# Kernel optimization log

Measured on AMD Instinct MI355X. Metric: run time of the kernel, lower is better.

## Reference

```python
import jax, jax.numpy as jnp
import numpy as np

B, N, E, H = 2048, 256, 32, 64
DIN = N + 2 * E  # masked_x + self_emb + parent_emb


def _lin_init(k, fan_in, fan_out):
    return jax.random.normal(k, (fan_in, fan_out), jnp.float32) / np.sqrt(fan_in).astype(np.float32)


def setup_inputs() -> dict:
    key = jax.random.key(0)
    ks = jax.random.split(key, 8)
    return {
        "x": jax.random.normal(ks[0], (B, N), jnp.float32),
        "adjacency": jax.random.uniform(ks[1], (N, N), jnp.float32),
        "embeddings": 0.01 * jax.random.normal(ks[2], (N, E), jnp.float32),
        "W1": _lin_init(ks[3], DIN, H), "b1": jnp.zeros((H,), jnp.float32),
        "g1": jnp.ones((H,), jnp.float32), "bt1": jnp.zeros((H,), jnp.float32),
        "W2": _lin_init(ks[4], H, H), "b2": jnp.zeros((H,), jnp.float32),
        "g2": jnp.ones((H,), jnp.float32), "bt2": jnp.zeros((H,), jnp.float32),
        "W3": _lin_init(ks[5], H, 2), "b3": jnp.zeros((2,), jnp.float32),
    }


def _layernorm(h, g, b, eps=1e-5):
    m = h.mean(-1, keepdims=True)
    v = h.var(-1, keepdims=True)
    return (h - m) / jnp.sqrt(v + eps) * g + b


def _leaky_relu(h):
    return jnp.where(h >= 0, h, 0.2 * h)


def reference(x, adjacency, embeddings, W1, b1, g1, bt1, W2, b2, g2, bt2, W3, b3):
    b, n = x.shape
    e = embeddings.shape[1]
    # masked_x[b,i,j] = adjacency[j,i] * x[b,j]  (per-node parent masking, vectorized over i)
    masked = x[:, None, :] * adjacency.T[None, :, :]            # (B, N, N)
    self_emb = jnp.broadcast_to(embeddings[None], (b, n, e))    # (B, N, E)
    # parent_weights[:, i] = adjacency[:, i] / (sum + 1e-8); parent_emb_i = pw_i @ embeddings
    pw = adjacency / (adjacency.sum(axis=0, keepdims=True) + 1e-8)
    parent_emb = jnp.broadcast_to((pw.T @ embeddings)[None], (b, n, e))  # (B, N, E)
    inp = jnp.concatenate([masked, self_emb, parent_emb], axis=-1)       # (B, N, N+2E)
    h = _leaky_relu(_layernorm(inp @ W1 + b1, g1, bt1))
    h = _leaky_relu(_layernorm(h @ W2 + b2, g2, bt2))
    out = h @ W3 + b3                                            # (B, N, 2)
    return out[..., 0], out[..., 1]  # (means, log_stds), each (B, N)
```

## Files before the change

kernel.cpp:

```cpp
#include <hip/hip_runtime.h>
#include <hip/hip_bf16.h>

#define BB 2048
#define NN 256
#define EE 32
#define HH 64

typedef __attribute__((ext_vector_type(8))) short s16x8;
typedef __attribute__((ext_vector_type(4))) short s16x4;
typedef __attribute__((ext_vector_type(4))) float f32x4;

__device__ __forceinline__ unsigned short f32_to_bf16_rne(float f) {
    __hip_bfloat16 h = __float2bfloat16(f);
    return *reinterpret_cast<unsigned short*>(&h);
}
__device__ __forceinline__ float bf16_to_f32(unsigned short h) {
    return __uint_as_float(((unsigned int)h) << 16);
}

__global__ __launch_bounds__(256) void prep_all(
    const float* __restrict__ x, const float* __restrict__ A,
    const float* __restrict__ emb, const float* __restrict__ W1,
    const float* __restrict__ b1, const float* __restrict__ W2,
    unsigned short* __restrict__ xh, unsigned short* __restrict__ xl,
    unsigned short* __restrict__ w2h, unsigned short* __restrict__ w2l,
    float* __restrict__ c) {

    __shared__ float aS[NN];
    __shared__ float red[256];
    __shared__ float peS[EE];

    const int bid = blockIdx.x;
    const int t   = threadIdx.x;

    if (bid < 512) {
        const int i4 = (bid * 256 + t) * 4;
        const f32x4 v = *(const f32x4*)(x + i4);
        s16x4 hv, lv;
        #pragma unroll
        for (int q = 0; q < 4; ++q) {
            const unsigned short hb = f32_to_bf16_rne(v[q]);
            hv[q] = (short)hb;
            lv[q] = (short)f32_to_bf16_rne(v[q] - bf16_to_f32(hb));
        }
        *(s16x4*)(xh + i4) = hv;
        *(s16x4*)(xl + i4) = lv;
    } else if (bid < 528) {
        const int idx = (bid - 512) * 256 + t;
        const int n = idx >> 6, k = idx & 63;
        const float w = W2[k * HH + n];
        const unsigned short hb = f32_to_bf16_rne(w);
        w2h[n * HH + k] = hb;
        w2l[n * HH + k] = f32_to_bf16_rne(w - bf16_to_f32(hb));
    } else {
        const int i = bid - 528;
        const float a_t = A[t * NN + i];
        aS[t] = a_t;
        red[t] = a_t;
        __syncthreads();
        #pragma unroll
        for (int s = 128; s > 0; s >>= 1) {
            if (t < s) red[t] += red[t + s];
            __syncthreads();
        }
        const float inv = 1.f / (red[0] + 1e-8f);

        const int e = t & 31, jg = t >> 5;
        float part = 0.f;
        #pragma unroll 8
        for (int r = 0; r < 32; ++r) {
            const int j = jg * 32 + r;
            part = fmaf(aS[j], emb[j * EE + e], part);
        }
        __syncthreads();
        red[t] = part;
        __syncthreads();
        if (t < 32) {
            float pe = 0.f;
            #pragma unroll
            for (int g = 0; g < 8; ++g) pe += red[g * 32 + t];
            peS[t] = pe * inv;
        }
        __syncthreads();

        if (t < HH) {
            float ch = b1[t];
            const float* embi = emb + i * EE;
            #pragma unroll 8
            for (int e2 = 0; e2 < EE; ++e2) {
                ch = fmaf(embi[e2], W1[(NN      + e2) * HH + t], ch);
                ch = fmaf(peS[e2],  W1[(NN + EE + e2) * HH + t], ch);
            }
            c[i * HH + t] = ch;
        }
    }
}

__global__ __launch_bounds__(256, 2) void fused_main(
    const unsigned short* __restrict__ xh, const unsigned short* __restrict__ xl,
    const float* __restrict__ A, const float* __restrict__ W1,
    const float* __restrict__ c,
    const unsigned short* __restrict__ w2h, const unsigned short* __restrict__ w2l,
    const float* __restrict__ g1, const float* __restrict__ bt1,
    const float* __restrict__ b2,
    const float* __restrict__ g2, const float* __restrict__ bt2,
    const float* __restrict__ W3, const float* __restrict__ b3,
    float* __restrict__ out) {

    __shared__ float smem[16384];
    __shared__ float aS[NN];
    unsigned short* Bh = (unsigned short*)smem;
    unsigned short* Bl = Bh + 32 * 512;
    float* tr = smem;
    unsigned short* Ah = (unsigned short*)smem;
    unsigned short* Al = Ah + 32 * 512;

    const int t  = threadIdx.x;
    const int i  = blockIdx.x & 255;
    const int b0 = (blockIdx.x >> 8) * 256;

    const int l  = t & 63;
    const int wv = t >> 6;
    const int lg = l >> 4;
    const int lm = l & 15;

    aS[t] = A[t * NN + i];
    __syncthreads();

    #pragma unroll
    for (int fr = 0; fr < 8; ++fr) {
        const int f  = wv * 8 + fr;
        const int kb = f >> 2, nt = f & 3;
        const int h  = nt * 16 + lm;
        const int jb = kb * 32 + lg * 8;
        s16x8 hv, lv;
        #pragma unroll
        for (int w = 0; w < 8; ++w) {
            const int j = jb + w;
            const float pw = aS[j] * W1[j * HH + h];
            const unsigned short hb = f32_to_bf16_rne(pw);
            hv[w] = (short)hb;
            lv[w] = (short)f32_to_bf16_rne(pw - bf16_to_f32(hb));
        }
        *(s16x8*)(Bh + f * 512 + l * 8) = hv;
        *(s16x8*)(Bl + f * 512 + l * 8) = lv;
    }
    __syncthreads();

    f32x4 acc[4][4];
    #pragma unroll
    for (int rt = 0; rt < 4; ++rt)
        #pragma unroll
        for (int nt = 0; nt < 4; ++nt) {
            acc[rt][nt][0] = 0.f; acc[rt][nt][1] = 0.f;
            acc[rt][nt][2] = 0.f; acc[rt][nt][3] = 0.f;
        }

    const int rowbase = b0 + wv * 64;
    for (int kb = 0; kb < 8; ++kb) {
        s16x8 bh[4], bl[4];
        #pragma unroll
        for (int nt = 0; nt < 4; ++nt) {
            const int sbase = ((kb * 4 + nt) * 64 + l) * 8;
            bh[nt] = *(const s16x8*)(Bh + sbase);
            bl[nt] = *(const s16x8*)(Bl + sbase);
        }
        const int koff = kb * 32 + lg * 8;
        #pragma unroll
        for (int rt = 0; rt < 4; ++rt) {
            const int row = rowbase + rt * 16 + lm;
            const s16x8 ah = *(const s16x8*)(xh + row * NN + koff);
            const s16x8 al = *(const s16x8*)(xl + row * NN + koff);
            #pragma unroll
            for (int nt = 0; nt < 4; ++nt) {
                acc[rt][nt] = __builtin_amdgcn_mfma_f32_16x16x32_bf16(ah, bh[nt], acc[rt][nt], 0, 0, 0);
                acc[rt][nt] = __builtin_amdgcn_mfma_f32_16x16x32_bf16(ah, bl[nt], acc[rt][nt], 0, 0, 0);
                acc[rt][nt] = __builtin_amdgcn_mfma_f32_16x16x32_bf16(al, bh[nt], acc[rt][nt], 0, 0, 0);
            }
        }
    }
    __syncthreads();

    #pragma unroll
    for (int rt = 0; rt < 4; ++rt)
        #pragma unroll
        for (int nt = 0; nt < 4; ++nt)
            #pragma unroll
            for (int rr = 0; rr < 4; ++rr) {
                const int wr  = wv * 64 + rt * 16 + lg * 4 + rr;
                const int col = nt * 16 + lm;
                const int q   = col >> 2;
                tr[wr * 64 + (((q ^ (wr & 15)) << 2) | (col & 3))] = acc[rt][nt][rr];
            }
    __syncthreads();

    float acc1[HH];
    #pragma unroll
    for (int q = 0; q < 16; ++q) {
        const f32x4 v = *(const f32x4*)&tr[t * 64 + ((q ^ (t & 15)) << 2)];
        acc1[4*q+0] = v[0]; acc1[4*q+1] = v[1]; acc1[4*q+2] = v[2]; acc1[4*q+3] = v[3];
    }
    __syncthreads();

    {
        const float* crow = c + i * HH;
        #pragma unroll
        for (int h = 0; h < HH; ++h) acc1[h] += crow[h];
    }
    {
        float m0 = 0.f, m1 = 0.f, m2 = 0.f, m3 = 0.f;
        #pragma unroll
        for (int h = 0; h < HH; h += 4) { m0 += acc1[h]; m1 += acc1[h+1]; m2 += acc1[h+2]; m3 += acc1[h+3]; }
        const float m = (m0 + m1 + m2 + m3) * (1.f / HH);
        float v0 = 0.f, v1 = 0.f, v2 = 0.f, v3 = 0.f;
        #pragma unroll
        for (int h = 0; h < HH; h += 4) {
            float d0 = acc1[h] - m, d1 = acc1[h+1] - m, d2 = acc1[h+2] - m, d3 = acc1[h+3] - m;
            v0 = fmaf(d0, d0, v0); v1 = fmaf(d1, d1, v1); v2 = fmaf(d2, d2, v2); v3 = fmaf(d3, d3, v3);
        }
        const float var = (v0 + v1 + v2 + v3) * (1.f / HH);
        const float inv = rsqrtf(var + 1e-5f);
        #pragma unroll
        for (int h = 0; h < HH; ++h) {
            float u = (acc1[h] - m) * inv * g1[h] + bt1[h];
            acc1[h] = (u >= 0.f) ? u : 0.2f * u;
        }
    }

    {
        const int f2base = (t >> 4) * 2;
        const int lm2    = t & 15;
        #pragma unroll
        for (int w = 0; w < 8; ++w) {
            const int kk = w >> 2, lg2 = w & 3;
            s16x8 hv, lv;
            #pragma unroll
            for (int e = 0; e < 8; ++e) {
                const float v = acc1[w * 8 + e];
                const unsigned short hb = f32_to_bf16_rne(v);
                hv[e] = (short)hb;
                lv[e] = (short)f32_to_bf16_rne(v - bf16_to_f32(hb));
            }
            const int base = (f2base + kk) * 512 + (lg2 * 16 + lm2) * 8;
            *(s16x8*)(Ah + base) = hv;
            *(s16x8*)(Al + base) = lv;
        }
    }
    __syncthreads();

    f32x4 acc2[4][4];
    #pragma unroll
    for (int rt = 0; rt < 4; ++rt)
        #pragma unroll
        for (int nt = 0; nt < 4; ++nt) {
            acc2[rt][nt][0] = 0.f; acc2[rt][nt][1] = 0.f;
            acc2[rt][nt][2] = 0.f; acc2[rt][nt][3] = 0.f;
        }
    #pragma unroll
    for (int kk = 0; kk < 2; ++kk) {
        s16x8 b2h[4], b2l[4];
        #pragma unroll
        for (int nt = 0; nt < 4; ++nt) {
            const int off = (nt * 16 + lm) * HH + kk * 32 + lg * 8;
            b2h[nt] = *(const s16x8*)(w2h + off);
            b2l[nt] = *(const s16x8*)(w2l + off);
        }
        #pragma unroll
        for (int rt = 0; rt < 4; ++rt) {
            const int base = ((wv * 4 + rt) * 2 + kk) * 512 + l * 8;
            const s16x8 a2h = *(const s16x8*)(Ah + base);
            const s16x8 a2l = *(const s16x8*)(Al + base);
            #pragma unroll
            for (int nt = 0; nt < 4; ++nt) {
                acc2[rt][nt] = __builtin_amdgcn_mfma_f32_16x16x32_bf16(a2h, b2h[nt], acc2[rt][nt], 0, 0, 0);
                acc2[rt][nt] = __builtin_amdgcn_mfma_f32_16x16x32_bf16(a2h, b2l[nt], acc2[rt][nt], 0, 0, 0);
                acc2[rt][nt] = __builtin_amdgcn_mfma_f32_16x16x32_bf16(a2l, b2h[nt], acc2[rt][nt], 0, 0, 0);
            }
        }
    }
    __syncthreads();

    #pragma unroll
    for (int rt = 0; rt < 4; ++rt)
        #pragma unroll
        for (int nt = 0; nt < 4; ++nt)
            #pragma unroll
            for (int rr = 0; rr < 4; ++rr) {
                const int wr  = wv * 64 + rt * 16 + lg * 4 + rr;
                const int col = nt * 16 + lm;
                const int q   = col >> 2;
                tr[wr * 64 + (((q ^ (wr & 15)) << 2) | (col & 3))] = acc2[rt][nt][rr];
            }
    __syncthreads();

    float accE[HH];
    #pragma unroll
    for (int q = 0; q < 16; ++q) {
        const f32x4 v = *(const f32x4*)&tr[t * 64 + ((q ^ (t & 15)) << 2)];
        accE[4*q+0] = v[0]; accE[4*q+1] = v[1]; accE[4*q+2] = v[2]; accE[4*q+3] = v[3];
    }
    #pragma unroll
    for (int h = 0; h < HH; ++h) accE[h] += b2[h];

    {
        float m0 = 0.f, m1 = 0.f, m2 = 0.f, m3 = 0.f;
        #pragma unroll
        for (int h = 0; h < HH; h += 4) { m0 += accE[h]; m1 += accE[h+1]; m2 += accE[h+2]; m3 += accE[h+3]; }
        const float m = (m0 + m1 + m2 + m3) * (1.f / HH);
        float v0 = 0.f, v1 = 0.f, v2 = 0.f, v3 = 0.f;
        #pragma unroll
        for (int h = 0; h < HH; h += 4) {
            float d0 = accE[h] - m, d1 = accE[h+1] - m, d2 = accE[h+2] - m, d3 = accE[h+3] - m;
            v0 = fmaf(d0, d0, v0); v1 = fmaf(d1, d1, v1); v2 = fmaf(d2, d2, v2); v3 = fmaf(d3, d3, v3);
        }
        const float var = (v0 + v1 + v2 + v3) * (1.f / HH);
        const float inv = rsqrtf(var + 1e-5f);
        #pragma unroll
        for (int h = 0; h < HH; ++h) {
            float u = (accE[h] - m) * inv * g2[h] + bt2[h];
            accE[h] = (u >= 0.f) ? u : 0.2f * u;
        }
    }

    float o0 = b3[0], o1 = b3[1];
    #pragma unroll
    for (int h = 0; h < HH; ++h) {
        o0 = fmaf(accE[h], W3[h * 2 + 0], o0);
        o1 = fmaf(accE[h], W3[h * 2 + 1], o1);
    }

    const int row = (b0 + t) * NN + i;
    out[row] = o0;
    out[BB * NN + row] = o1;
}

extern "C" void kernel_launch(void* const* d_in, const int* in_sizes, int n_in,
                              void* d_out, int out_size, void* d_ws, size_t ws_size,
                              hipStream_t stream) {
    const float* x   = (const float*)d_in[0];
    const float* A   = (const float*)d_in[1];
    const float* emb = (const float*)d_in[2];
    const float* W1  = (const float*)d_in[3];
    const float* b1  = (const float*)d_in[4];
    const float* g1  = (const float*)d_in[5];
    const float* bt1 = (const float*)d_in[6];
    const float* W2  = (const float*)d_in[7];
    const float* b2  = (const float*)d_in[8];
    const float* g2  = (const float*)d_in[9];
    const float* bt2 = (const float*)d_in[10];
    const float* W3  = (const float*)d_in[11];
    const float* b3  = (const float*)d_in[12];
    float* out = (float*)d_out;

    float* c = (float*)d_ws;
    unsigned short* xhp = (unsigned short*)(c + NN * HH);
    unsigned short* xlp = xhp + BB * NN;
    unsigned short* w2hp = xlp + BB * NN;
    unsigned short* w2lp = w2hp + HH * HH;

    prep_all<<<784, 256, 0, stream>>>(x, A, emb, W1, b1, W2,
                                      xhp, xlp, w2hp, w2lp, c);
    fused_main<<<NN * (BB / 256), 256, 0, stream>>>(
        xhp, xlp, A, W1, c, w2hp, w2lp, g1, bt1, b2, g2, bt2, W3, b3, out);
}
```

Baseline: 191.1 us.

## Do layernorms in MFMA register layout with shuffles, skip LDS round-trips

Both LayerNorm+LeakyReLU stages and the final W3 projection now run directly on the MFMA accumulator fragments, with row reductions done by 16-lane xor shuffles. This removes the per-thread LDS transpose back to row-per-thread form and the separate hi/lo bf16 staging buffers. The second GEMM now reads layer-1 activations from the swizzled fp32 tile in LDS and splits them into bf16 hi/lo on the fly, which removes several block barriers. The cost is many extra cross-lane shuffles and the extra register pressure of holding the fragment-shaped statistics.

```diff
diff --git a/kernel.cpp b/kernel.cpp
--- a/kernel.cpp
+++ b/kernel.cpp
@@ -112,8 +112,6 @@
     unsigned short* Bh = (unsigned short*)smem;
     unsigned short* Bl = Bh + 32 * 512;
     float* tr = smem;
-    unsigned short* Ah = (unsigned short*)smem;
-    unsigned short* Al = Ah + 32 * 512;
 
     const int t  = threadIdx.x;
     const int i  = blockIdx.x & 255;
@@ -179,6 +177,57 @@
             }
         }
     }
+
+    float cr[4], g1r[4], bt1r[4];
+    #pragma unroll
+    for (int nt = 0; nt < 4; ++nt) {
+        const int h = nt * 16 + lm;
+        cr[nt]   = c[i * HH + h];
+        g1r[nt]  = g1[h];
+        bt1r[nt] = bt1[h];
+    }
+    #pragma unroll
+    for (int rt = 0; rt < 4; ++rt)
+        #pragma unroll
+        for (int nt = 0; nt < 4; ++nt)
+            #pragma unroll
+            for (int rr = 0; rr < 4; ++rr)
+                acc[rt][nt][rr] += cr[nt];
+
+    float mm[4][4], iv[4][4];
+    #pragma unroll
+    for (int rt = 0; rt < 4; ++rt)
+        #pragma unroll
+        for (int rr = 0; rr < 4; ++rr) {
+            float s = acc[rt][0][rr] + acc[rt][1][rr] + acc[rt][2][rr] + acc[rt][3][rr];
+            s += __shfl_xor(s, 1); s += __shfl_xor(s, 2);
+            s += __shfl_xor(s, 4); s += __shfl_xor(s, 8);
+            mm[rt][rr] = s * 0.015625f;
+        }
+    #pragma unroll
+    for (int rt = 0; rt < 4; ++rt)
+        #pragma unroll
+        for (int rr = 0; rr < 4; ++rr) {
+            float v = 0.f;
+            #pragma unroll
+            for (int nt = 0; nt < 4; ++nt) {
+                const float d = acc[rt][nt][rr] - mm[rt][rr];
+                v = fmaf(d, d, v);
+            }
+            v += __shfl_xor(v, 1); v += __shfl_xor(v, 2);
+            v += __shfl_xor(v, 4); v += __shfl_xor(v, 8);
+            iv[rt][rr] = rsqrtf(v * 0.015625f + 1e-5f);
+        }
+    #pragma unroll
+    for (int rt = 0; rt < 4; ++rt)
+        #pragma unroll
+        for (int nt = 0; nt < 4; ++nt)
+            #pragma unroll
+            for (int rr = 0; rr < 4; ++rr) {
+                const float u = (acc[rt][nt][rr] - mm[rt][rr]) * iv[rt][rr] * g1r[nt] + bt1r[nt];
+                acc[rt][nt][rr] = (u >= 0.f) ? u : 0.2f * u;
+            }
+
     __syncthreads();
 
     #pragma unroll
@@ -192,61 +241,6 @@
                 const int q   = col >> 2;
                 tr[wr * 64 + (((q ^ (wr & 15)) << 2) | (col & 3))] = acc[rt][nt][rr];
             }
-    __syncthreads();
-
-    float acc1[HH];
-    #pragma unroll
-    for (int q = 0; q < 16; ++q) {
-        const f32x4 v = *(const f32x4*)&tr[t * 64 + ((q ^ (t & 15)) << 2)];
-        acc1[4*q+0] = v[0]; acc1[4*q+1] = v[1]; acc1[4*q+2] = v[2]; acc1[4*q+3] = v[3];
-    }
-    __syncthreads();
-
-    {
-        const float* crow = c + i * HH;
-        #pragma unroll
-        for (int h = 0; h < HH; ++h) acc1[h] += crow[h];
-    }
-    {
-        float m0 = 0.f, m1 = 0.f, m2 = 0.f, m3 = 0.f;
-        #pragma unroll
-        for (int h = 0; h < HH; h += 4) { m0 += acc1[h]; m1 += acc1[h+1]; m2 += acc1[h+2]; m3 += acc1[h+3]; }
-        const float m = (m0 + m1 + m2 + m3) * (1.f / HH);
-        float v0 = 0.f, v1 = 0.f, v2 = 0.f, v3 = 0.f;
-        #pragma unroll
-        for (int h = 0; h < HH; h += 4) {
-            float d0 = acc1[h] - m, d1 = acc1[h+1] - m, d2 = acc1[h+2] - m, d3 = acc1[h+3] - m;
-            v0 = fmaf(d0, d0, v0); v1 = fmaf(d1, d1, v1); v2 = fmaf(d2, d2, v2); v3 = fmaf(d3, d3, v3);
-        }
-        const float var = (v0 + v1 + v2 + v3) * (1.f / HH);
-        const float inv = rsqrtf(var + 1e-5f);
-        #pragma unroll
-        for (int h = 0; h < HH; ++h) {
-            float u = (acc1[h] - m) * inv * g1[h] + bt1[h];
-            acc1[h] = (u >= 0.f) ? u : 0.2f * u;
-        }
-    }
-
-    {
-        const int f2base = (t >> 4) * 2;
-        const int lm2    = t & 15;
-        #pragma unroll
-        for (int w = 0; w < 8; ++w) {
-            const int kk = w >> 2, lg2 = w & 3;
-            s16x8 hv, lv;
-            #pragma unroll
-            for (int e = 0; e < 8; ++e) {
-                const float v = acc1[w * 8 + e];
-                const unsigned short hb = f32_to_bf16_rne(v);
-                hv[e] = (short)hb;
-                lv[e] = (short)f32_to_bf16_rne(v - bf16_to_f32(hb));
-            }
-            const int base = (f2base + kk) * 512 + (lg2 * 16 + lm2) * 8;
-            *(s16x8*)(Ah + base) = hv;
-            *(s16x8*)(Al + base) = lv;
-        }
-    }
-    __syncthreads();
 
     f32x4 acc2[4][4];
     #pragma unroll
@@ -258,80 +252,112 @@
         }
     #pragma unroll
     for (int kk = 0; kk < 2; ++kk) {
-        s16x8 b2h[4], b2l[4];
+        s16x8 b2hf[4], b2lf[4];
         #pragma unroll
         for (int nt = 0; nt < 4; ++nt) {
             const int off = (nt * 16 + lm) * HH + kk * 32 + lg * 8;
-            b2h[nt] = *(const s16x8*)(w2h + off);
-            b2l[nt] = *(const s16x8*)(w2l + off);
+            b2hf[nt] = *(const s16x8*)(w2h + off);
+            b2lf[nt] = *(const s16x8*)(w2l + off);
         }
         #pragma unroll
         for (int rt = 0; rt < 4; ++rt) {
-            const int base = ((wv * 4 + rt) * 2 + kk) * 512 + l * 8;
-            const s16x8 a2h = *(const s16x8*)(Ah + base);
-            const s16x8 a2l = *(const s16x8*)(Al + base);
-            #pragma unroll
-            for (int nt = 0; nt < 4; ++nt) {
-                acc2[rt][nt] = __builtin_amdgcn_mfma_f32_16x16x32_bf16(a2h, b2h[nt], acc2[rt][nt], 0, 0, 0);
-                acc2[rt][nt] = __builtin_amdgcn_mfma_f32_16x16x32_bf16(a2h, b2l[nt], acc2[rt][nt], 0, 0, 0);
-                acc2[rt][nt] = __builtin_amdgcn_mfma_f32_16x16x32_bf16(a2l, b2h[nt], acc2[rt][nt], 0, 0, 0);
-            }
-        }
-    }
-    __syncthreads();
-
+            const int R   = wv * 64 + rt * 16 + lm;
+            const int swz = R & 15;
+            const int q0  = kk * 8 + lg * 2;
+            const f32x4 va = *(const f32x4*)&tr[R * 64 + (((q0    ) ^ swz) << 2)];
+            const f32x4 vb = *(const f32x4*)&tr[R * 64 + (((q0 + 1) ^ swz) << 2)];
+            s16x8 a2h, a2l;
+            #pragma unroll
+            for (int e = 0; e < 4; ++e) {
+                unsigned short hb = f32_to_bf16_rne(va[e]);
+                a2h[e]     = (short)hb;
+                a2l[e]     = (short)f32_to_bf16_rne(va[e] - bf16_to_f32(hb));
+                hb = f32_to_bf16_rne(vb[e]);
+                a2h[4 + e] = (short)hb;
+                a2l[4 + e] = (short)f32_to_bf16_rne(vb[e] - bf16_to_f32(hb));
+            }
+            #pragma unroll
+            for (int nt = 0; nt < 4; ++nt) {
+                acc2[rt][nt] = __builtin_amdgcn_mfma_f32_16x16x32_bf16(a2h, b2hf[nt], acc2[rt][nt], 0, 0, 0);
+                acc2[rt][nt] = __builtin_amdgcn_mfma_f32_16x16x32_bf16(a2h, b2lf[nt], acc2[rt][nt], 0, 0, 0);
+                acc2[rt][nt] = __builtin_amdgcn_mfma_f32_16x16x32_bf16(a2l, b2hf[nt], acc2[rt][nt], 0, 0, 0);
+            }
+        }
+    }
+
+    float b2r[4], g2r[4], bt2r[4], w30[4], w31[4];
+    #pragma unroll
+    for (int nt = 0; nt < 4; ++nt) {
+        const int h = nt * 16 + lm;
+        b2r[nt]  = b2[h];
+        g2r[nt]  = g2[h];
+        bt2r[nt] = bt2[h];
+        w30[nt]  = W3[h * 2 + 0];
+        w31[nt]  = W3[h * 2 + 1];
+    }
     #pragma unroll
     for (int rt = 0; rt < 4; ++rt)
         #pragma unroll
         for (int nt = 0; nt < 4; ++nt)
             #pragma unroll
-            for (int rr = 0; rr < 4; ++rr) {
-                const int wr  = wv * 64 + rt * 16 + lg * 4 + rr;
-                const int col = nt * 16 + lm;
-                const int q   = col >> 2;
-                tr[wr * 64 + (((q ^ (wr & 15)) << 2) | (col & 3))] = acc2[rt][nt][rr];
-            }
-    __syncthreads();
-
-    float accE[HH];
-    #pragma unroll
-    for (int q = 0; q < 16; ++q) {
-        const f32x4 v = *(const f32x4*)&tr[t * 64 + ((q ^ (t & 15)) << 2)];
-        accE[4*q+0] = v[0]; accE[4*q+1] = v[1]; accE[4*q+2] = v[2]; accE[4*q+3] = v[3];
-    }
-    #pragma unroll
-    for (int h = 0; h < HH; ++h) accE[h] += b2[h];
-
-    {
-        float m0 = 0.f, m1 = 0.f, m2 = 0.f, m3 = 0.f;
-        #pragma unroll
-        for (int h = 0; h < HH; h += 4) { m0 += accE[h]; m1 += accE[h+1]; m2 += accE[h+2]; m3 += accE[h+3]; }
-        const float m = (m0 + m1 + m2 + m3) * (1.f / HH);
-        float v0 = 0.f, v1 = 0.f, v2 = 0.f, v3 = 0.f;
-        #pragma unroll
-        for (int h = 0; h < HH; h += 4) {
-            float d0 = accE[h] - m, d1 = accE[h+1] - m, d2 = accE[h+2] - m, d3 = accE[h+3] - m;
-            v0 = fmaf(d0, d0, v0); v1 = fmaf(d1, d1, v1); v2 = fmaf(d2, d2, v2); v3 = fmaf(d3, d3, v3);
-        }
-        const float var = (v0 + v1 + v2 + v3) * (1.f / HH);
-        const float inv = rsqrtf(var + 1e-5f);
-        #pragma unroll
-        for (int h = 0; h < HH; ++h) {
-            float u = (accE[h] - m) * inv * g2[h] + bt2[h];
-            accE[h] = (u >= 0.f) ? u : 0.2f * u;
-        }
-    }
-
-    float o0 = b3[0], o1 = b3[1];
-    #pragma unroll
-    for (int h = 0; h < HH; ++h) {
-        o0 = fmaf(accE[h], W3[h * 2 + 0], o0);
-        o1 = fmaf(accE[h], W3[h * 2 + 1], o1);
-    }
-
-    const int row = (b0 + t) * NN + i;
-    out[row] = o0;
-    out[BB * NN + row] = o1;
+            for (int rr = 0; rr < 4; ++rr)
+                acc2[rt][nt][rr] += b2r[nt];
+
+    #pragma unroll
+    for (int rt = 0; rt < 4; ++rt)
+        #pragma unroll
+        for (int rr = 0; rr < 4; ++rr) {
+            float s = acc2[rt][0][rr] + acc2[rt][1][rr] + acc2[rt][2][rr] + acc2[rt][3][rr];
+            s += __shfl_xor(s, 1); s += __shfl_xor(s, 2);
+            s += __shfl_xor(s, 4); s += __shfl_xor(s, 8);
+            mm[rt][rr] = s * 0.015625f;
+        }
+    #pragma unroll
+    for (int rt = 0; rt < 4; ++rt)
+        #pragma unroll
+        for (int rr = 0; rr < 4; ++rr) {
+            float v = 0.f;
+            #pragma unroll
+            for (int nt = 0; nt < 4; ++nt) {
+                const float d = acc2[rt][nt][rr] - mm[rt][rr];
+                v = fmaf(d, d, v);
+            }
+            v += __shfl_xor(v, 1); v += __shfl_xor(v, 2);
+            v += __shfl_xor(v, 4); v += __shfl_xor(v, 8);
+            iv[rt][rr] = rsqrtf(v * 0.015625f + 1e-5f);
+        }
+
+    float o0[4][4], o1[4][4];
+    #pragma unroll
+    for (int rt = 0; rt < 4; ++rt)
+        #pragma unroll
+        for (int rr = 0; rr < 4; ++rr) {
+            float p0 = 0.f, p1 = 0.f;
+            #pragma unroll
+            for (int nt = 0; nt < 4; ++nt) {
+                float u = (acc2[rt][nt][rr] - mm[rt][rr]) * iv[rt][rr] * g2r[nt] + bt2r[nt];
+                u = (u >= 0.f) ? u : 0.2f * u;
+                p0 = fmaf(u, w30[nt], p0);
+                p1 = fmaf(u, w31[nt], p1);
+            }
+            p0 += __shfl_xor(p0, 1); p0 += __shfl_xor(p0, 2);
+            p0 += __shfl_xor(p0, 4); p0 += __shfl_xor(p0, 8);
+            p1 += __shfl_xor(p1, 1); p1 += __shfl_xor(p1, 2);
+            p1 += __shfl_xor(p1, 4); p1 += __shfl_xor(p1, 8);
+            o0[rt][rr] = p0;
+            o1[rt][rr] = p1;
+        }
+
+    float so0 = 0.f, so1 = 0.f;
+    #pragma unroll
+    for (int rt = 0; rt < 4; ++rt)
+        #pragma unroll
+        for (int rr = 0; rr < 4; ++rr)
+            if (lm == rt * 4 + rr) { so0 = o0[rt][rr]; so1 = o1[rt][rr]; }
+
+    const int rowg = b0 + wv * 64 + (lm >> 2) * 16 + lg * 4 + (lm & 3);
+    out[rowg * NN + i]           = so0 + b3[0];
+    out[BB * NN + rowg * NN + i] = so1 + b3[1];
 }
 
 extern "C" void kernel_launch(void* const* d_in, const int* in_sizes, int n_in,
```

New measurement: 201.0 us. 1.05x slower.
